# Performance work log

Hardware: AMD Instinct MI355X
Metric: run time of the kernel (lower is better)

Reference implementation:

```python
import jax, jax.numpy as jnp
import numpy as np

SEG = 512        # segment_size
DIL = 2          # dilation_rate
LN_EPS = 1e-5


def _layer_norm(x, gamma, beta):
    mu = jnp.mean(x, axis=-1, keepdims=True)
    var = jnp.var(x, axis=-1, keepdims=True)
    return (x - mu) * jax.lax.rsqrt(var + LN_EPS) * gamma + beta


def setup_inputs() -> dict:
    key = jax.random.key(0)
    ks = jax.random.split(key, 5)
    B, N, D = 4, 4096, 1024
    s = 0.02
    return {
        "x": jax.random.normal(ks[0], (B, N, D), dtype=jnp.float32),
        "Wq": jax.random.normal(ks[1], (D, D), dtype=jnp.float32) * s,
        "Wk": jax.random.normal(ks[2], (D, D), dtype=jnp.float32) * s,
        "Wv": jax.random.normal(ks[3], (D, D), dtype=jnp.float32) * s,
        "Wo": jax.random.normal(ks[4], (D, D), dtype=jnp.float32) * s,
        "gamma": jnp.ones((D,), dtype=jnp.float32),
        "beta": jnp.zeros((D,), dtype=jnp.float32),
    }


def reference(x, Wq, Wk, Wv, Wo, gamma, beta):
    B, N, D = x.shape
    n_seg = N // SEG
    s = SEG // DIL  # tokens per segment after dilation
    # strided dilated gather: [B, n_seg, s, D]
    xs = x.reshape(B, n_seg, SEG, D)[:, :, ::DIL, :]
    # torch Linear(bias=False): x @ W.T ; then LayerNorm on each of q,k,v
    q = _layer_norm(jnp.einsum('bgsd,ed->bgse', xs, Wq), gamma, beta)
    k = _layer_norm(jnp.einsum('bgsd,ed->bgse', xs, Wk), gamma, beta)
    v = _layer_norm(jnp.einsum('bgsd,ed->bgse', xs, Wv), gamma, beta)
    # causal SDPA with head_dim = D (no head split in the original code)
    scale = 1.0 / jnp.sqrt(jnp.asarray(D, dtype=q.dtype))
    scores = jnp.einsum('bgqd,bgkd->bgqk', q, k) * scale  # [B, n_seg, s, s]
    causal = jnp.tril(jnp.ones((s, s), dtype=bool))
    scores = jnp.where(causal, scores, jnp.finfo(scores.dtype).min)
    attn = jax.nn.softmax(scores, axis=-1)
    y = jnp.einsum('bgqk,bgkd->bgqd', attn, v)  # [B, n_seg, s, D]
    y = y.reshape(B, N // DIL, D)
    # strided scatter into zero-initialized full tensor
    y_full = jnp.zeros((B, N, D), dtype=y.dtype).at[:, ::DIL, :].set(y)
    out = jnp.einsum('bnd,ed->bne', y_full, Wo)
    return out
```

## Files before the change

### kernel.cpp

```cpp
#include <hip/hip_runtime.h>
#include <stdint.h>

typedef __bf16 bf16_t;
typedef __bf16 bf16x8 __attribute__((ext_vector_type(8)));
typedef __bf16 bf16x4 __attribute__((ext_vector_type(4)));
typedef float  f32x4  __attribute__((ext_vector_type(4)));


__device__ __forceinline__ void gload16(const void* g, void* lds)
{
    __builtin_amdgcn_global_load_lds(
        (__attribute__((address_space(1))) void*)(void*)g,
        (__attribute__((address_space(3))) void*)lds,
        16, 0, 0);
}

__device__ __forceinline__ f32x4 mfma16(bf16x8 a, bf16x8 b, f32x4 c)
{
    return __builtin_amdgcn_mfma_f32_16x16x32_bf16(a, b, c, 0, 0, 0);
}

#define SBAR()   asm volatile("s_barrier" ::: "memory")
#define LGKM0()  asm volatile("s_waitcnt lgkmcnt(0)" ::: "memory")
#define VMCNT(N) asm volatile("s_waitcnt vmcnt(" #N ")" ::: "memory")


__global__ __launch_bounds__(256)
void prep_kernel(const float* __restrict__ Wq, const float* __restrict__ Wk,
                 const float* __restrict__ Wv, const float* __restrict__ Wo,
                 const float* __restrict__ x,
                 bf16_t* __restrict__ Wqkv, bf16_t* __restrict__ Wob,
                 bf16_t* __restrict__ Xe)
{
    const int bid = blockIdx.x;
    const int t = threadIdx.x;
    if (bid < 4096) {
        const int which = bid >> 10;
        const int blk = bid & 1023;
        const float* src = which == 0 ? Wq : which == 1 ? Wk : which == 2 ? Wv : Wo;
        bf16_t* dst = which == 3 ? Wob : Wqkv + (size_t)which * 1048576;
        const size_t i = ((size_t)blk * 256 + t) * 4;
        float4 f = *(const float4*)&src[i];
        bf16x4 o;
        o[0] = (bf16_t)f.x; o[1] = (bf16_t)f.y; o[2] = (bf16_t)f.z; o[3] = (bf16_t)f.w;
        *(bf16x4*)&dst[i] = o;
    } else {
        const int m = bid - 4096;
        const int b = m >> 11, g = (m >> 8) & 7, j = m & 255;
        const float* src = x + ((size_t)b * 4096 + g * 512 + 2 * j) * 1024;
        bf16_t* dst = Xe + (size_t)m * 1024;
        float4 f = *(const float4*)&src[t * 4];
        bf16x4 o;
        o[0] = (bf16_t)f.x; o[1] = (bf16_t)f.y; o[2] = (bf16_t)f.z; o[3] = (bf16_t)f.w;
        *(bf16x4*)&dst[t * 4] = o;
    }
}

template<int EPI, int NSUB>
__global__ __launch_bounds__(512, 2)
void gemm_mt(const bf16_t* __restrict__ A, const bf16_t* __restrict__ B,
             void* __restrict__ Cv, int lda, int ldb, int ldc)
{
    __shared__ __align__(16) char lds[98304];

    const int tid = threadIdx.x;
    const int w = tid >> 6, lane = tid & 63;
    const int wr = w >> 2, wc = w & 3;
    const int fr = lane & 15, fg = lane >> 4;

    const int lin = blockIdx.y * 8 + blockIdx.x;
    const int L = (lin & 7) * 32 + (lin >> 3);
    const int bm = L >> 3, j = L & 7;
    const int NT = NSUB * 16;

    const int s = tid ^ ((tid >> 3) & 7);
    const char* srcA  = (const char*)A + ((size_t)(bm * 256 + (s >> 3)) * lda + (s & 7) * 8) * 2;
    const char* srcB0 = (const char*)B + ((size_t)(j * NSUB * 128 + (s >> 3)) * ldb + (s & 7) * 8) * 2;
    const size_t aStep  = (size_t)64 * lda * 2;
    const size_t bStep  = (size_t)64 * ldb * 2;
    const size_t bnStep = (size_t)128 * ldb * 2;
    const int ldsW = w * 1024;

#define STG_A(T, Q) gload16(srcA + (Q) * aStep + (size_t)((T) & 15) * 128,          \
                            lds + ((T) & 1) * 49152 + (Q) * 8192 + ldsW)
#define STG_B(T, U) gload16(srcB0 + (size_t)((T) >> 4) * bnStep + (U) * bStep       \
                                  + (size_t)((T) & 15) * 128,                        \
                            lds + ((T) & 1) * 49152 + 32768 + (U) * 8192 + ldsW)

    const int flip = (fr & 7) << 4;
    const int aoff = (wr * 128 + fr) * 128 + fg * 16;
    const int boff = 32768 + (wc * 32 + fr) * 128 + fg * 16;

    bf16x8 a[4][2], b[2][2];
    f32x4 acc[8][2] = {};

#define LDA(PH, CB) do {                                                        \
    _Pragma("unroll") for (int mi = 0; mi < 4; ++mi)                            \
    _Pragma("unroll") for (int ks = 0; ks < 2; ++ks)                            \
        a[mi][ks] = *(const bf16x8*)(lds + (CB) +                               \
            ((aoff + (PH) * 8192 + mi * 2048 + ks * 64) ^ flip));               \
} while (0)

#define LDB(CB) do {                                                            \
    _Pragma("unroll") for (int ni = 0; ni < 2; ++ni)                            \
    _Pragma("unroll") for (int ks = 0; ks < 2; ++ks)                            \
        b[ni][ks] = *(const bf16x8*)(lds + (CB) +                               \
            ((boff + ni * 2048 + ks * 64) ^ flip));                             \
} while (0)

#define MF(PH) do {                                                             \
    _Pragma("unroll") for (int mi = 0; mi < 4; ++mi)                            \
    _Pragma("unroll") for (int ni = 0; ni < 2; ++ni)                            \
    _Pragma("unroll") for (int ks = 0; ks < 2; ++ks)                            \
        acc[(PH) * 4 + mi][ni] =                                                \
            mfma16(b[ni][ks], a[mi][ks], acc[(PH) * 4 + mi][ni]);               \
} while (0)

    const int r0 = bm * 256 + wr * 128 + fr;
    const int c0w = wc * 32 + fg * 4;

#define DO_EPI(SUB) do {                                                                  \
    const int _c0 = (j * NSUB + (SUB)) * 128 + c0w;                                       \
    if constexpr (EPI == 0) {                                                             \
        bf16_t* C = (bf16_t*)Cv;                                                          \
        _Pragma("unroll") for (int mig = 0; mig < 8; ++mig)                               \
        _Pragma("unroll") for (int ni = 0; ni < 2; ++ni) {                                \
            const int row = r0 + (mig >> 2) * 64 + (mig & 3) * 16;                        \
            bf16x4 o;                                                                     \
            _Pragma("unroll") for (int r = 0; r < 4; ++r) o[r] = (bf16_t)acc[mig][ni][r]; \
            *(bf16x4*)&C[(size_t)row * ldc + _c0 + ni * 16] = o;                          \
        }                                                                                 \
    } else {                                                                              \
        float* C = (float*)Cv;                                                            \
        const f32x4 z4 = {0.f, 0.f, 0.f, 0.f};                                            \
        _Pragma("unroll") for (int mig = 0; mig < 8; ++mig)                               \
        _Pragma("unroll") for (int ni = 0; ni < 2; ++ni) {                                \
            const int m  = r0 + (mig >> 2) * 64 + (mig & 3) * 16;                         \
            const int gr = ((m >> 11) << 12) | (((m >> 8) & 7) << 9) | ((m & 255) << 1);  \
            *(f32x4*)&C[(size_t)gr * 1024 + _c0 + ni * 16]       = acc[mig][ni];          \
            *(f32x4*)&C[(size_t)(gr + 1) * 1024 + _c0 + ni * 16] = z4;                    \
        }                                                                                 \
    }                                                                                     \
    _Pragma("unroll") for (int mig = 0; mig < 8; ++mig)                                   \
    _Pragma("unroll") for (int ni = 0; ni < 2; ++ni)                                      \
        acc[mig][ni] = (f32x4){0.f, 0.f, 0.f, 0.f};                                       \
} while (0)

    STG_A(0, 0); STG_A(0, 1); STG_A(0, 2); STG_A(0, 3); STG_B(0, 0); STG_B(0, 1);
    STG_A(1, 0); STG_A(1, 2); STG_B(1, 0); STG_B(1, 1);
    VMCNT(4);
    SBAR();

    for (int t = 0; t < NT - 2; ++t) {
        const int cb = (t & 1) * 49152;
        LDA(0, cb); LDB(cb);
        STG_A(t + 1, 1); STG_A(t + 1, 3);
        SBAR(); LGKM0();
        __builtin_amdgcn_s_setprio(1); MF(0); __builtin_amdgcn_s_setprio(0);
        VMCNT(6);
        SBAR();
        LDA(1, cb);
        STG_A(t + 2, 0); STG_A(t + 2, 2); STG_B(t + 2, 0); STG_B(t + 2, 1);
        SBAR(); LGKM0();
        __builtin_amdgcn_s_setprio(1); MF(1); __builtin_amdgcn_s_setprio(0);
        VMCNT(6);
        if ((t & 15) == 15) DO_EPI(t >> 4);
        SBAR();
    }

    {
        const int cb = ((NT - 2) & 1) * 49152;
        LDA(0, cb); LDB(cb);
        STG_A(NT - 1, 1); STG_A(NT - 1, 3);
        SBAR(); LGKM0();
        MF(0);
        VMCNT(6);
        SBAR();
        LDA(1, cb);
        SBAR(); LGKM0();
        MF(1);
        VMCNT(0);
        SBAR();
    }
    {
        const int cb = ((NT - 1) & 1) * 49152;
        LDA(0, cb); LDB(cb);
        LGKM0();
        MF(0);
        LDA(1, cb);
        LGKM0();
        MF(1);
    }
    DO_EPI(NSUB - 1);

#undef STG_A
#undef STG_B
#undef LDA
#undef LDB
#undef MF
#undef DO_EPI
}

template<int EPI>
__global__ __launch_bounds__(256)
void gemm_nt(const bf16_t* __restrict__ A, const bf16_t* __restrict__ B,
             void* __restrict__ Cv,
             int K, int lda, int ldb, int ldc,
             long sA, long sB, long sC, int flags)
{
    __shared__ __align__(16) bf16_t Asm[128 * 32];
    __shared__ __align__(16) bf16_t Bsm[128 * 32];

    const int bn = blockIdx.x, bm = blockIdx.y, bz = blockIdx.z;
    const int tid  = threadIdx.x;
    const int wave = tid >> 6;
    const int lane = tid & 63;
    const int wr = wave >> 1, wc = wave & 1;

    const bf16_t* Ab = A + (long)bz * sA;
    const bf16_t* Bb = B + (long)bz * sB;

    const int Keff = ((flags & 1) && bm == 0) ? (K >> 1) : K;

    const int sw0 = tid ^ ((tid >> 3) & 3);
    const int dd1 = tid + 256;
    const int sw1 = dd1 ^ ((dd1 >> 3) & 3);
    const bf16_t* a0 = Ab + (size_t)(bm * 128 + (sw0 >> 2)) * lda + (sw0 & 3) * 8;
    const bf16_t* a1 = Ab + (size_t)(bm * 128 + (sw1 >> 2)) * lda + (sw1 & 3) * 8;
    const bf16_t* b0 = Bb + (size_t)(bn * 128 + (sw0 >> 2)) * ldb + (sw0 & 3) * 8;
    const bf16_t* b1 = Bb + (size_t)(bn * 128 + (sw1 >> 2)) * ldb + (sw1 & 3) * 8;
    char* ldsA = (char*)Asm + wave * 1024;
    char* ldsB = (char*)Bsm + wave * 1024;

    f32x4 acc[4][4] = {};

    const int frow = lane & 15;
    const int fk   = (lane >> 4) * 8;
    const int flip = (frow & 6) << 2;

    for (int k0 = 0; k0 < Keff; k0 += 32) {
        gload16(a0, ldsA);
        gload16(a1, ldsA + 4096);
        gload16(b0, ldsB);
        gload16(b1, ldsB + 4096);
        a0 += 32; a1 += 32; b0 += 32; b1 += 32;
        __syncthreads();

        bf16x8 af[4], bfr[4];
#pragma unroll
        for (int mi = 0; mi < 4; ++mi)
            af[mi] = *(const bf16x8*)&Asm[(size_t)(((wr * 64 + mi * 16 + frow) * 32 + fk) ^ flip)];
#pragma unroll
        for (int ni = 0; ni < 4; ++ni)
            bfr[ni] = *(const bf16x8*)&Bsm[(size_t)(((wc * 64 + ni * 16 + frow) * 32 + fk) ^ flip)];
#pragma unroll
        for (int mi = 0; mi < 4; ++mi)
#pragma unroll
            for (int ni = 0; ni < 4; ++ni)
                acc[mi][ni] = mfma16(bfr[ni], af[mi], acc[mi][ni]);
        __syncthreads();
    }

    const int row0 = bm * 128 + wr * 64 + frow;
    const int col0 = bn * 128 + wc * 64 + (lane >> 4) * 4;

    if constexpr (EPI == 0) {
        bf16_t* C = (bf16_t*)Cv + (long)bz * sC;
#pragma unroll
        for (int mi = 0; mi < 4; ++mi)
#pragma unroll
            for (int ni = 0; ni < 4; ++ni) {
                bf16x4 o;
#pragma unroll
                for (int r = 0; r < 4; ++r) o[r] = (bf16_t)acc[mi][ni][r];
                *(bf16x4*)&C[(size_t)(row0 + mi * 16) * ldc + col0 + ni * 16] = o;
            }
    } else {
        float* C = (float*)Cv + (long)bz * sC;
#pragma unroll
        for (int mi = 0; mi < 4; ++mi)
#pragma unroll
            for (int ni = 0; ni < 4; ++ni)
                *(f32x4*)&C[(size_t)(row0 + mi * 16) * ldc + col0 + ni * 16] = acc[mi][ni];
    }
}

__global__ __launch_bounds__(256)
void qk_tr_kernel(const bf16_t* __restrict__ qkv, float* __restrict__ Smat,
                  bf16_t* __restrict__ Vt)
{
    __shared__ __align__(16) char smem[16384];
    const int bid = blockIdx.x;
    const int tid = threadIdx.x;

    if (bid < 96) {
        const int seg = bid / 3, r = bid % 3;
        const int bm = (r + 1) >> 1, bn = r >> 1;
        const bf16_t* Ab = qkv + (size_t)seg * 256 * 3072;
        const bf16_t* Bb = Ab + 1024;
        bf16_t* Asm = (bf16_t*)smem;
        bf16_t* Bsm = Asm + 4096;

        const int wave = tid >> 6, lane = tid & 63;
        const int wr = wave >> 1, wc = wave & 1;
        const int sw0 = tid ^ ((tid >> 3) & 3);
        const int dd1 = tid + 256;
        const int sw1 = dd1 ^ ((dd1 >> 3) & 3);
        const bf16_t* a0 = Ab + (size_t)(bm * 128 + (sw0 >> 2)) * 3072 + (sw0 & 3) * 8;
        const bf16_t* a1 = Ab + (size_t)(bm * 128 + (sw1 >> 2)) * 3072 + (sw1 & 3) * 8;
        const bf16_t* b0 = Bb + (size_t)(bn * 128 + (sw0 >> 2)) * 3072 + (sw0 & 3) * 8;
        const bf16_t* b1 = Bb + (size_t)(bn * 128 + (sw1 >> 2)) * 3072 + (sw1 & 3) * 8;
        char* ldsA = (char*)Asm + wave * 1024;
        char* ldsB = (char*)Bsm + wave * 1024;

        f32x4 acc[4][4] = {};
        const int frow = lane & 15;
        const int fk   = (lane >> 4) * 8;
        const int flip = (frow & 6) << 2;

        for (int k0 = 0; k0 < 1024; k0 += 32) {
            gload16(a0, ldsA);
            gload16(a1, ldsA + 4096);
            gload16(b0, ldsB);
            gload16(b1, ldsB + 4096);
            a0 += 32; a1 += 32; b0 += 32; b1 += 32;
            __syncthreads();

            bf16x8 af[4], bfr[4];
#pragma unroll
            for (int mi = 0; mi < 4; ++mi)
                af[mi] = *(const bf16x8*)&Asm[(size_t)(((wr * 64 + mi * 16 + frow) * 32 + fk) ^ flip)];
#pragma unroll
            for (int ni = 0; ni < 4; ++ni)
                bfr[ni] = *(const bf16x8*)&Bsm[(size_t)(((wc * 64 + ni * 16 + frow) * 32 + fk) ^ flip)];
#pragma unroll
            for (int mi = 0; mi < 4; ++mi)
#pragma unroll
                for (int ni = 0; ni < 4; ++ni)
                    acc[mi][ni] = mfma16(bfr[ni], af[mi], acc[mi][ni]);
            __syncthreads();
        }

        float* C = Smat + (size_t)seg * 65536;
        const int row0 = bm * 128 + wr * 64 + frow;
        const int col0 = bn * 128 + wc * 64 + (lane >> 4) * 4;
#pragma unroll
        for (int mi = 0; mi < 4; ++mi)
#pragma unroll
            for (int ni = 0; ni < 4; ++ni)
                *(f32x4*)&C[(size_t)(row0 + mi * 16) * 256 + col0 + ni * 16] = acc[mi][ni];
    } else {
        const int id2 = bid - 96;
        const int seg = id2 >> 6;
        const int rem = id2 & 63;
        const int eb = rem >> 2, kb = rem & 3;
        bf16_t* tile = (bf16_t*)smem;

        const int rr = tid >> 2, cs = (tid & 3) * 16;
        const bf16_t* src = qkv + ((size_t)(seg * 256 + kb * 64 + rr)) * 3072
                                + 2048 + eb * 64 + cs;
        bf16x8 v0 = *(const bf16x8*)&src[0];
        bf16x8 v1 = *(const bf16x8*)&src[8];
#pragma unroll
        for (int i = 0; i < 8; ++i) {
            tile[rr * 65 + cs + i]     = v0[i];
            tile[rr * 65 + cs + 8 + i] = v1[i];
        }
        __syncthreads();
        bf16x8 o0, o1;
#pragma unroll
        for (int i = 0; i < 8; ++i) {
            o0[i] = tile[(cs + i) * 65 + rr];
            o1[i] = tile[(cs + 8 + i) * 65 + rr];
        }
        bf16_t* dst = Vt + (size_t)seg * 262144 + (size_t)(eb * 64 + rr) * 256 + kb * 64 + cs;
        *(bf16x8*)&dst[0] = o0;
        *(bf16x8*)&dst[8] = o1;
    }
}

__global__ __launch_bounds__(256)
void ln_kernel(bf16_t* __restrict__ qkv,
               const float* __restrict__ gamma, const float* __restrict__ beta)
{
    const int t = threadIdx.x;
    const int r = t >> 7;
    const int row = blockIdx.x * 2 + r;
    const int which = blockIdx.y;
    bf16_t* p = qkv + (size_t)row * 3072 + which * 1024;
    const int li = t & 127;
    const int c0 = li * 8;

    bf16x8 v = *(const bf16x8*)&p[c0];
    float f[8];
    float s = 0.f, ss = 0.f;
#pragma unroll
    for (int i = 0; i < 8; ++i) { f[i] = (float)v[i]; s += f[i]; ss += f[i] * f[i]; }
#pragma unroll
    for (int o = 32; o; o >>= 1) { s += __shfl_xor(s, o); ss += __shfl_xor(ss, o); }

    __shared__ float rs_[4], rss_[4];
    const int wave = t >> 6, lane = t & 63;
    if (lane == 0) { rs_[wave] = s; rss_[wave] = ss; }
    __syncthreads();
    s  = rs_[2 * r] + rs_[2 * r + 1];
    ss = rss_[2 * r] + rss_[2 * r + 1];

    const float mu   = s * (1.f / 1024.f);
    const float var  = ss * (1.f / 1024.f) - mu * mu;
    const float rstd = rsqrtf(var + 1e-5f);

    bf16x8 o;
#pragma unroll
    for (int i = 0; i < 8; ++i)
        o[i] = (bf16_t)((f[i] - mu) * rstd * gamma[c0 + i] + beta[c0 + i]);
    *(bf16x8*)&p[c0] = o;
}

__global__ __launch_bounds__(256)
void softmax_kernel(const float* __restrict__ S, bf16_t* __restrict__ P)
{
    const int q = blockIdx.x & 255;
    const size_t base = (size_t)blockIdx.x * 256;
    const int c = threadIdx.x;
    const bool ok = (c <= q);

    float v = ok ? S[base + c] * (1.f / 32.f) : -3.0e38f;
    float m = v;
#pragma unroll
    for (int o = 32; o; o >>= 1) m = fmaxf(m, __shfl_xor(m, o));

    __shared__ float rm[4], rsum[4];
    const int wave = c >> 6, lane = c & 63;
    if (lane == 0) rm[wave] = m;
    __syncthreads();
    m = fmaxf(fmaxf(rm[0], rm[1]), fmaxf(rm[2], rm[3]));

    float e = ok ? __expf(v - m) : 0.f;
    float s = e;
#pragma unroll
    for (int o = 32; o; o >>= 1) s += __shfl_xor(s, o);
    if (lane == 0) rsum[wave] = s;
    __syncthreads();
    s = rsum[0] + rsum[1] + rsum[2] + rsum[3];

    P[base + c] = (bf16_t)(e / s);
}


extern "C" void kernel_launch(void* const* d_in, const int* in_sizes, int n_in,
                              void* d_out, int out_size, void* d_ws, size_t ws_size,
                              hipStream_t stream)
{
    const float* x     = (const float*)d_in[0];
    const float* Wq    = (const float*)d_in[1];
    const float* Wk    = (const float*)d_in[2];
    const float* Wv    = (const float*)d_in[3];
    const float* Wo    = (const float*)d_in[4];
    const float* gamma = (const float*)d_in[5];
    const float* beta  = (const float*)d_in[6];
    float* out = (float*)d_out;

    char* ws = (char*)d_ws;
    bf16_t* Xe   = (bf16_t*)(ws);
    bf16_t* Wqkv = (bf16_t*)(ws + (16u  << 20));
    bf16_t* Wob  = (bf16_t*)(ws + (22u  << 20));
    bf16_t* QKV  = (bf16_t*)(ws + (24u  << 20));
    float*  Smat = (float*) (ws + (72u  << 20));
    bf16_t* P    = (bf16_t*)(ws + (80u  << 20));
    bf16_t* Vt   = (bf16_t*)(ws + (84u  << 20));
    bf16_t* Y    = (bf16_t*)(ws + (100u << 20));

    prep_kernel<<<12288, 256, 0, stream>>>(Wq, Wk, Wv, Wo, x, Wqkv, Wob, Xe);

    gemm_mt<0, 3><<<dim3(8, 32), 512, 0, stream>>>(
        Xe, Wqkv, QKV, 1024, 1024, 3072);

    ln_kernel<<<dim3(4096, 3), 256, 0, stream>>>(QKV, gamma, beta);

    qk_tr_kernel<<<96 + 2048, 256, 0, stream>>>(QKV, Smat, Vt);

    softmax_kernel<<<8192, 256, 0, stream>>>(Smat, P);

    gemm_nt<0><<<dim3(8, 2, 32), 256, 0, stream>>>(
        P, Vt, Y, 256, 256, 256, 1024,
        65536L, 262144L, 262144L, 1);

    gemm_mt<2, 1><<<dim3(8, 32), 512, 0, stream>>>(
        Y, Wob, out, 1024, 1024, 1024);
}
```

Before: 173.8 us.

## Replace QKV projection GEMM with 256x256-tile pipelined MFMA kernel

Adds a new gemm256 kernel that computes 256x256 output tiles with 8 waves, a double-buffered 128KB LDS staging scheme built on global_load_lds, XOR-swizzled LDS reads, and interleaved quarter-tile loads and MFMAs with s_setprio around the MFMA blocks. It replaces the previous gemm_mt<0,3> launch for the fused QKV projection (8192x3072x1024) with a 12x32 grid. The larger tile is meant to raise arithmetic intensity and overlap memory with compute. The cost is 128KB of LDS per block, which may limit occupancy to one block per CU despite the launch bounds.

```diff
diff --git a/kernel.cpp b/kernel.cpp
--- a/kernel.cpp
+++ b/kernel.cpp
@@ -54,6 +54,142 @@
         o[0] = (bf16_t)f.x; o[1] = (bf16_t)f.y; o[2] = (bf16_t)f.z; o[3] = (bf16_t)f.w;
         *(bf16x4*)&dst[t * 4] = o;
     }
+}
+
+__global__ __launch_bounds__(512, 2)
+void gemm256(const bf16_t* __restrict__ A, const bf16_t* __restrict__ B,
+             bf16_t* __restrict__ C, int K, int lda, int ldb, int ldc)
+{
+    __shared__ __align__(16) char lds[131072];
+
+    const int tid = threadIdx.x;
+    const int w = tid >> 6, lane = tid & 63;
+    const int wr = w >> 2, wc = w & 3;
+    const int fr = lane & 15, fg = lane >> 4;
+    const int NT = K >> 6;
+
+    const int lin = blockIdx.y * gridDim.x + blockIdx.x;
+    const int nwg = gridDim.x * gridDim.y;
+    const int cpx = nwg >> 3;
+    const int L = (lin & 7) * cpx + (lin >> 3);
+    const int bn = L % gridDim.x, bm = L / gridDim.x;
+
+    const int d0 = tid, d1 = 512 + tid;
+    const int s0 = d0 ^ ((d0 >> 3) & 7);
+    const int s1 = d1 ^ ((d1 >> 3) & 7);
+    const size_t fixA0 = ((size_t)(bm * 256 + (s0 >> 9) * 128 + ((s0 >> 3) & 63)) * lda + (s0 & 7) * 8) * 2;
+    const size_t fixA1 = ((size_t)(bm * 256 + (s1 >> 9) * 128 + ((s1 >> 3) & 63)) * lda + (s1 & 7) * 8) * 2;
+    const size_t fixB0 = ((size_t)(bn * 256 + (s0 >> 8) * 64 + ((s0 >> 3) & 31)) * ldb + (s0 & 7) * 8) * 2;
+    const size_t fixB1 = ((size_t)(bn * 256 + (s1 >> 8) * 64 + ((s1 >> 3) & 31)) * ldb + (s1 & 7) * 8) * 2;
+    const size_t mqStep = (size_t)64 * lda * 2;
+    const size_t nqStep = (size_t)32 * ldb * 2;
+    const char* Ac = (const char*)A;
+    const char* Bc = (const char*)B;
+    const int ldsW = w * 1024;
+
+#define STAGE(T, ISB, Q) do {                                                     \
+    const int _b = ((T) & 1) * 65536 + (ISB) * 32768 + (Q) * 16384 + ldsW;        \
+    const char *_g0, *_g1;                                                        \
+    if (ISB) { _g0 = Bc + (Q)*nqStep + fixB0 + (size_t)(T)*128;                   \
+               _g1 = Bc + (Q)*nqStep + fixB1 + (size_t)(T)*128; }                 \
+    else     { _g0 = Ac + (Q)*mqStep + fixA0 + (size_t)(T)*128;                   \
+               _g1 = Ac + (Q)*mqStep + fixA1 + (size_t)(T)*128; }                 \
+    gload16(_g0, lds + _b);                                                       \
+    gload16(_g1, lds + _b + 8192);                                                \
+} while (0)
+
+    const int abase = wr * 8192 + fr * 128 + fg * 16;
+    const int bbase = wc * 4096 + fr * 128 + fg * 16;
+    const int flip  = (fr & 7) << 4;
+
+    bf16x8 a[4][2], b0[2][2], b1[2][2];
+    f32x4 acc[8][4] = {};
+
+#define LOAD_A(MQ, CB) do {                                                                 \
+    _Pragma("unroll") for (int mi = 0; mi < 4; ++mi)                                        \
+    _Pragma("unroll") for (int ks = 0; ks < 2; ++ks)                                        \
+        a[mi][ks] = *(const bf16x8*)(lds + (CB) + (MQ)*16384 +                              \
+                                     ((abase + mi*2048 + ks*64) ^ flip));                   \
+} while (0)
+
+#define LOAD_B(REG, NQ, CB) do {                                                            \
+    _Pragma("unroll") for (int ni = 0; ni < 2; ++ni)                                        \
+    _Pragma("unroll") for (int ks = 0; ks < 2; ++ks)                                        \
+        REG[ni][ks] = *(const bf16x8*)(lds + (CB) + 32768 + (NQ)*16384 +                    \
+                                       ((bbase + ni*2048 + ks*64) ^ flip));                 \
+} while (0)
+
+#define MFMA_Q(MQ, REG, NQ) do {                                                            \
+    _Pragma("unroll") for (int mi = 0; mi < 4; ++mi)                                        \
+    _Pragma("unroll") for (int ni = 0; ni < 2; ++ni)                                        \
+    _Pragma("unroll") for (int ks = 0; ks < 2; ++ks)                                        \
+        acc[(MQ)*4+mi][(NQ)*2+ni] =                                                         \
+            mfma16(REG[ni][ks], a[mi][ks], acc[(MQ)*4+mi][(NQ)*2+ni]);                      \
+} while (0)
+
+    STAGE(0, 0, 0); STAGE(0, 1, 0); STAGE(0, 1, 1); STAGE(0, 0, 1);
+    VMCNT(4);
+    STAGE(1, 0, 0); STAGE(1, 1, 0); STAGE(1, 1, 1);
+    VMCNT(6);
+    SBAR();
+
+    for (int t = 0; t < NT - 2; ++t) {
+        const int cb = (t & 1) * 65536;
+        LOAD_A(0, cb); LOAD_B(b0, 0, cb);
+        STAGE(t + 1, 0, 1);
+        SBAR(); LGKM0();
+        __builtin_amdgcn_s_setprio(1); MFMA_Q(0, b0, 0); __builtin_amdgcn_s_setprio(0);
+        SBAR();
+        LOAD_B(b1, 1, cb);
+        STAGE(t + 2, 0, 0);
+        SBAR(); LGKM0();
+        __builtin_amdgcn_s_setprio(1); MFMA_Q(0, b1, 1); __builtin_amdgcn_s_setprio(0);
+        SBAR();
+        LOAD_A(1, cb);
+        STAGE(t + 2, 1, 0);
+        SBAR(); LGKM0();
+        __builtin_amdgcn_s_setprio(1); MFMA_Q(1, b1, 1); __builtin_amdgcn_s_setprio(0);
+        SBAR();
+        STAGE(t + 2, 1, 1);
+        SBAR();
+        __builtin_amdgcn_s_setprio(1); MFMA_Q(1, b0, 0); __builtin_amdgcn_s_setprio(0);
+        VMCNT(6);
+        SBAR();
+    }
+
+    STAGE(NT - 1, 0, 1);
+    VMCNT(0);
+    SBAR();
+    for (int t = NT - 2; t < NT; ++t) {
+        const int cb = (t & 1) * 65536;
+        LOAD_A(0, cb); LOAD_B(b0, 0, cb);
+        LGKM0();
+        MFMA_Q(0, b0, 0);
+        LOAD_B(b1, 1, cb);
+        LGKM0();
+        MFMA_Q(0, b1, 1);
+        LOAD_A(1, cb);
+        LGKM0();
+        MFMA_Q(1, b1, 1);
+        MFMA_Q(1, b0, 0);
+    }
+
+#undef STAGE
+#undef LOAD_A
+#undef LOAD_B
+#undef MFMA_Q
+
+    const int r0 = bm * 256 + wr * 128 + fr;
+    const int c0 = bn * 256 + wc * 64 + fg * 4;
+#pragma unroll
+    for (int mig = 0; mig < 8; ++mig)
+#pragma unroll
+        for (int nig = 0; nig < 4; ++nig) {
+            bf16x4 o;
+#pragma unroll
+            for (int r = 0; r < 4; ++r) o[r] = (bf16_t)acc[mig][nig][r];
+            *(bf16x4*)&C[(size_t)(r0 + mig * 16) * ldc + c0 + nig * 16] = o;
+        }
 }
 
 template<int EPI, int NSUB>
@@ -473,8 +609,7 @@
 
     prep_kernel<<<12288, 256, 0, stream>>>(Wq, Wk, Wv, Wo, x, Wqkv, Wob, Xe);
 
-    gemm_mt<0, 3><<<dim3(8, 32), 512, 0, stream>>>(
-        Xe, Wqkv, QKV, 1024, 1024, 3072);
+    gemm256<<<dim3(12, 32), 512, 0, stream>>>(Xe, Wqkv, QKV, 1024, 1024, 1024, 3072);
 
     ln_kernel<<<dim3(4096, 3), 256, 0, stream>>>(QKV, gamma, beta);
 
```

Result: slower. 179.3 us (+3.1%).

## Fuse causal softmax into QK^T kernel and drop fp32 score matrix

Applied to the files above, without the earlier changes.

QK^T blocks now compute full 128x256 (or 128x128 for the first causal half) score rows per workgroup with 512 threads, then apply scaling, causal masking, and softmax in registers with LDS cross-wave reductions, writing bf16 P directly. This removes the separate softmax launch and the fp32 score round trip through memory, and skips the fully masked upper-right tile. The number of QK blocks drops from 96 to 64, so each block does more work with less parallelism, and the V transpose path is reshaped for 512 threads.

```diff
diff --git a/kernel.cpp b/kernel.cpp
--- a/kernel.cpp
+++ b/kernel.cpp
@@ -285,97 +285,153 @@
     }
 }
 
-__global__ __launch_bounds__(256)
-void qk_tr_kernel(const bf16_t* __restrict__ qkv, float* __restrict__ Smat,
-                  bf16_t* __restrict__ Vt)
-{
-    __shared__ __align__(16) char smem[16384];
+template<int NI>
+__device__ __forceinline__ void qk_block(
+    const bf16_t* __restrict__ Ab, const bf16_t* __restrict__ Bb,
+    bf16_t* __restrict__ Pseg, int qb, char* smem, int tid)
+{
+    bf16_t* Asm = (bf16_t*)smem;
+    bf16_t* Bsm = (bf16_t*)(smem + 8192);
+    float*  red = (float*)(smem + 24576);
+
+    const int w = tid >> 6, lane = tid & 63;
+    const int wr = w >> 2, wc = w & 3;
+    const int frow = lane & 15, fg = lane >> 4;
+
+    const int g0 = tid, g1 = tid + 512;
+    const int s0 = g0 ^ ((g0 >> 3) & 3);
+    const int s1 = g1 ^ ((g1 >> 3) & 3);
+    const bf16_t* a0 = Ab + (size_t)(s0 >> 2) * 3072 + (s0 & 3) * 8;
+    const bf16_t* b0 = Bb + (size_t)(s0 >> 2) * 3072 + (s0 & 3) * 8;
+    const bf16_t* b1 = Bb + (size_t)(s1 >> 2) * 3072 + (s1 & 3) * 8;
+    char* ldsA = smem + w * 1024;
+    char* ldsB = smem + 8192 + w * 1024;
+
+    f32x4 acc[4][NI] = {};
+    const int fk = fg * 8;
+    const int flip = (frow & 6) << 2;
+    const int Nw = NI * 16;
+
+    for (int k0 = 0; k0 < 1024; k0 += 32) {
+        gload16(a0, ldsA);
+        gload16(b0, ldsB);
+        if (NI == 4) gload16(b1, ldsB + 8192);
+        a0 += 32; b0 += 32; b1 += 32;
+        __syncthreads();
+
+        bf16x8 af[4], bf_[NI];
+#pragma unroll
+        for (int mi = 0; mi < 4; ++mi)
+            af[mi] = *(const bf16x8*)&Asm[((wr * 64 + mi * 16 + frow) * 32 + fk) ^ flip];
+#pragma unroll
+        for (int ni = 0; ni < NI; ++ni)
+            bf_[ni] = *(const bf16x8*)&Bsm[((wc * Nw + ni * 16 + frow) * 32 + fk) ^ flip];
+#pragma unroll
+        for (int mi = 0; mi < 4; ++mi)
+#pragma unroll
+            for (int ni = 0; ni < NI; ++ni)
+                acc[mi][ni] = mfma16(bf_[ni], af[mi], acc[mi][ni]);
+        __syncthreads();
+    }
+
+    const int base_rloc = wr * 64 + frow;
+    const float scale = 1.0f / 32.0f;
+
+#pragma unroll
+    for (int mi = 0; mi < 4; ++mi) {
+        const int rl = base_rloc + mi * 16;
+        const int grow = qb * 128 + rl;
+        float m = -3.0e38f;
+#pragma unroll
+        for (int ni = 0; ni < NI; ++ni)
+#pragma unroll
+            for (int r = 0; r < 4; ++r) {
+                const int col = wc * Nw + ni * 16 + fg * 4 + r;
+                float v = acc[mi][ni][r] * scale;
+                if (col > grow) v = -3.0e38f;
+                acc[mi][ni][r] = v;
+                m = fmaxf(m, v);
+            }
+        m = fmaxf(m, __shfl_xor(m, 16));
+        m = fmaxf(m, __shfl_xor(m, 32));
+        if (fg == 0) red[rl * 4 + wc] = m;
+    }
+    __syncthreads();
+    float mx[4];
+#pragma unroll
+    for (int mi = 0; mi < 4; ++mi) {
+        const int rl = base_rloc + mi * 16;
+        mx[mi] = fmaxf(fmaxf(red[rl * 4 + 0], red[rl * 4 + 1]),
+                       fmaxf(red[rl * 4 + 2], red[rl * 4 + 3]));
+    }
+    __syncthreads();
+
+#pragma unroll
+    for (int mi = 0; mi < 4; ++mi) {
+        const int rl = base_rloc + mi * 16;
+        float s = 0.f;
+#pragma unroll
+        for (int ni = 0; ni < NI; ++ni)
+#pragma unroll
+            for (int r = 0; r < 4; ++r) {
+                const float e = __expf(acc[mi][ni][r] - mx[mi]);
+                acc[mi][ni][r] = e;
+                s += e;
+            }
+        s += __shfl_xor(s, 16);
+        s += __shfl_xor(s, 32);
+        if (fg == 0) red[rl * 4 + wc] = s;
+    }
+    __syncthreads();
+
+#pragma unroll
+    for (int mi = 0; mi < 4; ++mi) {
+        const int rl = base_rloc + mi * 16;
+        const float inv = 1.0f / (red[rl * 4 + 0] + red[rl * 4 + 1] +
+                                  red[rl * 4 + 2] + red[rl * 4 + 3]);
+        const int grow = qb * 128 + rl;
+#pragma unroll
+        for (int ni = 0; ni < NI; ++ni) {
+            bf16x4 o;
+#pragma unroll
+            for (int r = 0; r < 4; ++r) o[r] = (bf16_t)(acc[mi][ni][r] * inv);
+            *(bf16x4*)&Pseg[(size_t)grow * 256 + wc * Nw + ni * 16 + fg * 4] = o;
+        }
+    }
+}
+
+__global__ __launch_bounds__(512)
+void qk_sm_tr_kernel(const bf16_t* __restrict__ qkv, bf16_t* __restrict__ P,
+                     bf16_t* __restrict__ Vt)
+{
+    __shared__ __align__(16) char smem[26624];
     const int bid = blockIdx.x;
     const int tid = threadIdx.x;
 
-    if (bid < 96) {
-        const int seg = bid / 3, r = bid % 3;
-        const int bm = (r + 1) >> 1, bn = r >> 1;
-        const bf16_t* Ab = qkv + (size_t)seg * 256 * 3072;
-        const bf16_t* Bb = Ab + 1024;
-        bf16_t* Asm = (bf16_t*)smem;
-        bf16_t* Bsm = Asm + 4096;
-
-        const int wave = tid >> 6, lane = tid & 63;
-        const int wr = wave >> 1, wc = wave & 1;
-        const int sw0 = tid ^ ((tid >> 3) & 3);
-        const int dd1 = tid + 256;
-        const int sw1 = dd1 ^ ((dd1 >> 3) & 3);
-        const bf16_t* a0 = Ab + (size_t)(bm * 128 + (sw0 >> 2)) * 3072 + (sw0 & 3) * 8;
-        const bf16_t* a1 = Ab + (size_t)(bm * 128 + (sw1 >> 2)) * 3072 + (sw1 & 3) * 8;
-        const bf16_t* b0 = Bb + (size_t)(bn * 128 + (sw0 >> 2)) * 3072 + (sw0 & 3) * 8;
-        const bf16_t* b1 = Bb + (size_t)(bn * 128 + (sw1 >> 2)) * 3072 + (sw1 & 3) * 8;
-        char* ldsA = (char*)Asm + wave * 1024;
-        char* ldsB = (char*)Bsm + wave * 1024;
-
-        f32x4 acc[4][4] = {};
-        const int frow = lane & 15;
-        const int fk   = (lane >> 4) * 8;
-        const int flip = (frow & 6) << 2;
-
-        for (int k0 = 0; k0 < 1024; k0 += 32) {
-            gload16(a0, ldsA);
-            gload16(a1, ldsA + 4096);
-            gload16(b0, ldsB);
-            gload16(b1, ldsB + 4096);
-            a0 += 32; a1 += 32; b0 += 32; b1 += 32;
-            __syncthreads();
-
-            bf16x8 af[4], bfr[4];
-#pragma unroll
-            for (int mi = 0; mi < 4; ++mi)
-                af[mi] = *(const bf16x8*)&Asm[(size_t)(((wr * 64 + mi * 16 + frow) * 32 + fk) ^ flip)];
-#pragma unroll
-            for (int ni = 0; ni < 4; ++ni)
-                bfr[ni] = *(const bf16x8*)&Bsm[(size_t)(((wc * 64 + ni * 16 + frow) * 32 + fk) ^ flip)];
-#pragma unroll
-            for (int mi = 0; mi < 4; ++mi)
-#pragma unroll
-                for (int ni = 0; ni < 4; ++ni)
-                    acc[mi][ni] = mfma16(bfr[ni], af[mi], acc[mi][ni]);
-            __syncthreads();
-        }
-
-        float* C = Smat + (size_t)seg * 65536;
-        const int row0 = bm * 128 + wr * 64 + frow;
-        const int col0 = bn * 128 + wc * 64 + (lane >> 4) * 4;
-#pragma unroll
-        for (int mi = 0; mi < 4; ++mi)
-#pragma unroll
-            for (int ni = 0; ni < 4; ++ni)
-                *(f32x4*)&C[(size_t)(row0 + mi * 16) * 256 + col0 + ni * 16] = acc[mi][ni];
+    if (bid < 64) {
+        const int seg = bid >> 1, qb = bid & 1;
+        const bf16_t* Ab = qkv + (size_t)seg * 786432 + (size_t)qb * 128 * 3072;
+        const bf16_t* Bb = qkv + (size_t)seg * 786432 + 1024;
+        bf16_t* Pseg = P + (size_t)seg * 65536;
+        if (qb) qk_block<4>(Ab, Bb, Pseg, 1, smem, tid);
+        else    qk_block<2>(Ab, Bb, Pseg, 0, smem, tid);
     } else {
-        const int id2 = bid - 96;
+        const int id2 = bid - 64;
         const int seg = id2 >> 6;
         const int rem = id2 & 63;
         const int eb = rem >> 2, kb = rem & 3;
         bf16_t* tile = (bf16_t*)smem;
-
-        const int rr = tid >> 2, cs = (tid & 3) * 16;
-        const bf16_t* src = qkv + ((size_t)(seg * 256 + kb * 64 + rr)) * 3072
+        const int rr = tid >> 3, cs = (tid & 7) * 8;
+        const bf16_t* src = qkv + ((size_t)seg * 256 + kb * 64 + rr) * 3072
                                 + 2048 + eb * 64 + cs;
-        bf16x8 v0 = *(const bf16x8*)&src[0];
-        bf16x8 v1 = *(const bf16x8*)&src[8];
-#pragma unroll
-        for (int i = 0; i < 8; ++i) {
-            tile[rr * 65 + cs + i]     = v0[i];
-            tile[rr * 65 + cs + 8 + i] = v1[i];
-        }
+        bf16x8 v = *(const bf16x8*)src;
+#pragma unroll
+        for (int i = 0; i < 8; ++i) tile[rr * 65 + cs + i] = v[i];
         __syncthreads();
-        bf16x8 o0, o1;
-#pragma unroll
-        for (int i = 0; i < 8; ++i) {
-            o0[i] = tile[(cs + i) * 65 + rr];
-            o1[i] = tile[(cs + 8 + i) * 65 + rr];
-        }
-        bf16_t* dst = Vt + (size_t)seg * 262144 + (size_t)(eb * 64 + rr) * 256 + kb * 64 + cs;
-        *(bf16x8*)&dst[0] = o0;
-        *(bf16x8*)&dst[8] = o1;
+        bf16x8 o;
+#pragma unroll
+        for (int i = 0; i < 8; ++i) o[i] = tile[(cs + i) * 65 + rr];
+        *(bf16x8*)&Vt[(size_t)seg * 262144 + (size_t)(eb * 64 + rr) * 256 + kb * 64 + cs] = o;
     }
 }
 
@@ -415,36 +471,6 @@
     for (int i = 0; i < 8; ++i)
         o[i] = (bf16_t)((f[i] - mu) * rstd * gamma[c0 + i] + beta[c0 + i]);
     *(bf16x8*)&p[c0] = o;
-}
-
-__global__ __launch_bounds__(256)
-void softmax_kernel(const float* __restrict__ S, bf16_t* __restrict__ P)
-{
-    const int q = blockIdx.x & 255;
-    const size_t base = (size_t)blockIdx.x * 256;
-    const int c = threadIdx.x;
-    const bool ok = (c <= q);
-
-    float v = ok ? S[base + c] * (1.f / 32.f) : -3.0e38f;
-    float m = v;
-#pragma unroll
-    for (int o = 32; o; o >>= 1) m = fmaxf(m, __shfl_xor(m, o));
-
-    __shared__ float rm[4], rsum[4];
-    const int wave = c >> 6, lane = c & 63;
-    if (lane == 0) rm[wave] = m;
-    __syncthreads();
-    m = fmaxf(fmaxf(rm[0], rm[1]), fmaxf(rm[2], rm[3]));
-
-    float e = ok ? __expf(v - m) : 0.f;
-    float s = e;
-#pragma unroll
-    for (int o = 32; o; o >>= 1) s += __shfl_xor(s, o);
-    if (lane == 0) rsum[wave] = s;
-    __syncthreads();
-    s = rsum[0] + rsum[1] + rsum[2] + rsum[3];
-
-    P[base + c] = (bf16_t)(e / s);
 }
 
 
@@ -466,7 +492,6 @@
     bf16_t* Wqkv = (bf16_t*)(ws + (16u  << 20));
     bf16_t* Wob  = (bf16_t*)(ws + (22u  << 20));
     bf16_t* QKV  = (bf16_t*)(ws + (24u  << 20));
-    float*  Smat = (float*) (ws + (72u  << 20));
     bf16_t* P    = (bf16_t*)(ws + (80u  << 20));
     bf16_t* Vt   = (bf16_t*)(ws + (84u  << 20));
     bf16_t* Y    = (bf16_t*)(ws + (100u << 20));
@@ -478,9 +503,7 @@
 
     ln_kernel<<<dim3(4096, 3), 256, 0, stream>>>(QKV, gamma, beta);
 
-    qk_tr_kernel<<<96 + 2048, 256, 0, stream>>>(QKV, Smat, Vt);
-
-    softmax_kernel<<<8192, 256, 0, stream>>>(Smat, P);
+    qk_sm_tr_kernel<<<64 + 2048, 512, 0, stream>>>(QKV, P, Vt);
 
     gemm_nt<0><<<dim3(8, 2, 32), 256, 0, stream>>>(
         P, Vt, Y, 256, 256, 256, 1024,
```

After: 171.9 us. Within noise of the previous version (-1.1%).
